# Optimization experiments

Hardware: AMD Instinct MI355X
Metric: run time of the kernel (lower is better)

The kernel has to match this reference:

```python
import jax, jax.numpy as jnp
import numpy as np

B, T, I, H, O = 128, 1024, 128, 1024, 128

def setup_inputs() -> dict:
    key = jax.random.key(0)
    ks = jax.random.split(key, 11)
    s = 1.0 / np.sqrt(H)  # torch default LSTM init scale
    return {
        "x": jax.random.normal(ks[0], (B, T, I), jnp.float32),
        "sequence_length": jax.random.randint(ks[1], (B,), 0, T, jnp.int64 if jax.config.jax_enable_x64 else jnp.int32),
        "hn": jax.random.normal(ks[2], (B, H), jnp.float32),
        "cn": jax.random.normal(ks[3], (B, H), jnp.float32),
        "output_t": jax.random.normal(ks[4], (B, O), jnp.float32),
        "W_ih": jax.random.normal(ks[5], (4 * H, I + O), jnp.float32) * s,
        "W_hh": jax.random.normal(ks[6], (4 * H, H), jnp.float32) * s,
        "b_ih": jax.random.normal(ks[7], (4 * H,), jnp.float32) * s,
        "b_hh": jax.random.normal(ks[8], (4 * H,), jnp.float32) * s,
        "W_out": jax.random.normal(ks[9], (O, H), jnp.float32) * s,
        "b_out": jax.random.normal(ks[10], (O,), jnp.float32) * s,
    }

def reference(x, sequence_length, hn, cn, output_t, W_ih, W_hh, b_ih, b_hh, W_out, b_out):
    # eval mode (self.training=False): no dropout applied
    Tn = x.shape[1]
    Hd = hn.shape[-1]
    # masks[t, b] = 1.0 if sequence_length[b] > t
    masks = (jnp.arange(Tn)[:, None] < sequence_length[None, :]).astype(x.dtype)  # [T, B]
    xs = jnp.transpose(x, (1, 0, 2))  # [T, B, I]
    bias = b_ih + b_hh

    def step(carry, inp):
        h, c, out_t = carry
        xt, m = inp                      # xt [B,I], m [B]
        m = m[:, None]                   # [B,1]
        lstm_in = jnp.concatenate([xt * m, out_t], axis=-1)  # [B, I+O]
        gates = lstm_in @ W_ih.T + h @ W_hh.T + bias          # [B, 4H]
        i_g, f_g, g_g, o_g = jnp.split(gates, 4, axis=-1)     # torch gate order i,f,g,o
        i_g = jax.nn.sigmoid(i_g)
        f_g = jax.nn.sigmoid(f_g)
        g_g = jnp.tanh(g_g)
        o_g = jax.nn.sigmoid(o_g)
        c = f_g * c + i_g * g_g
        h = o_g * jnp.tanh(c)
        out_t = h @ W_out.T + b_out      # [B, O]
        return (h, c, out_t), out_t * m

    (_, _, _), ys = jax.lax.scan(step, (hn, cn, output_t), (xs, masks))
    return jnp.transpose(ys, (1, 0, 2))  # [B, T, O]
```

## Files before the change

### kernel.cpp

```cpp
#include <hip/hip_runtime.h>
#include <stdint.h>

#define Tn 1024
#define In 128

typedef __attribute__((ext_vector_type(8))) short short8;
typedef __attribute__((ext_vector_type(4))) float f32x4;
typedef unsigned long long u64;

#define WS_WFRAG  0ull
#define WS_WOUT   (WS_WFRAG + 10485760ull)
#define WS_Z0     (WS_WOUT + 262144ull)
#define WS_HBUF   (WS_Z0 + 32768ull)
#define WS_BIAS   (WS_HBUF + 524288ull)
#define WS_CNT    (WS_BIAS + 16384ull)

__device__ __forceinline__ unsigned short f2bf(float f) {
  unsigned u = __builtin_bit_cast(unsigned, f);
  return (unsigned short)((u + 0x7FFFu + ((u >> 16) & 1u)) >> 16);
}
__device__ __forceinline__ float fast_sig(float v) {
  float e = __builtin_amdgcn_exp2f(-1.44269504089f * v);
  return __builtin_amdgcn_rcpf(1.0f + e);
}
__device__ __forceinline__ float fast_tanh(float v) {
  float a = fabsf(v);
  float e = __builtin_amdgcn_exp2f(-2.88539008178f * a);
  float r = (1.0f - e) * __builtin_amdgcn_rcpf(1.0f + e);
  return copysignf(r, v);
}

__global__ void k_wfrag(const float* __restrict__ Wih, const float* __restrict__ Whh,
                        const float* __restrict__ Wout, char* __restrict__ ws) {
  const int u = blockIdx.x, nt = blockIdx.y, kt = blockIdx.z;
  const int lane = threadIdx.x;
  const int col = lane & 15, quad = lane >> 4;
  const int r = nt * 16 + col;
  const int g = r >> 5, jj = r & 31;
  const int n = g * 1024 + u * 32 + jj;
  float v[8];
  if (kt < 32) {
    const int k = kt * 32 + quad * 8;
    #pragma unroll
    for (int e = 0; e < 8; e++) v[e] = Whh[(size_t)n * 1024 + k + e];
    const float* wo = Wih + (size_t)n * 256 + 128;
    for (int o = 0; o < 128; o++) {
      const float wv = wo[o];
      const float* wr = Wout + (size_t)o * 1024 + k;
      #pragma unroll
      for (int e = 0; e < 8; e++) v[e] = fmaf(wv, wr[e], v[e]);
    }
  } else if (kt < 36) {
    const int k = (kt - 32) * 32 + quad * 8;
    #pragma unroll
    for (int e = 0; e < 8; e++) v[e] = Wih[(size_t)n * 256 + k + e];
  } else {
    const int o = (kt - 36) * 32 + quad * 8;
    #pragma unroll
    for (int e = 0; e < 8; e++) v[e] = Wih[(size_t)n * 256 + 128 + o + e];
  }
  short8 pk;
  #pragma unroll
  for (int e = 0; e < 8; e++) pk[e] = (short)f2bf(v[e]);
  *(short8*)(ws + WS_WFRAG + ((size_t)((u * 8 + nt) * 40 + kt) * 64 + lane) * 16) = pk;
}

__global__ void k_misc(const float* __restrict__ Wout, const float* __restrict__ hn,
                       const float* __restrict__ out_t, const float* __restrict__ bout,
                       const float* __restrict__ bih, const float* __restrict__ bhh,
                       const float* __restrict__ Wih, float* __restrict__ outp,
                       char* __restrict__ ws) {
  const int blk = blockIdx.x, lane = threadIdx.x;
  const int col = lane & 15, quad = lane >> 4;
  if (blk < 256) {
    const int u = blk >> 5, kt = blk & 31;
    const int o = u * 16 + col, j0 = kt * 32 + quad * 8;
    short8 pk;
    #pragma unroll
    for (int e = 0; e < 8; e++) pk[e] = (short)f2bf(Wout[(size_t)o * 1024 + j0 + e]);
    *(short8*)(ws + WS_WOUT + ((size_t)(u * 32 + kt) * 64 + lane) * 16) = pk;
  } else if (blk < 512) {
    const int t2 = blk - 256;
    const int mm = t2 >> 5, kt = t2 & 31;
    const int b = mm * 16 + col, j0 = kt * 32 + quad * 8;
    short8 pk;
    #pragma unroll
    for (int e = 0; e < 8; e++) pk[e] = (short)f2bf(hn[(size_t)b * 1024 + j0 + e]);
    *(short8*)(ws + WS_HBUF + ((size_t)((8 + mm) * 32 + kt) * 64 + lane) * 16) = pk;
  } else if (blk < 544) {
    const int t2 = blk - 512;
    const int mm = t2 >> 2, kz = t2 & 3;
    const int b = mm * 16 + col;
    const int o0 = kz * 32 + quad * 8;
    float acc[8];
    #pragma unroll
    for (int e = 0; e < 8; e++) acc[e] = out_t[(size_t)b * 128 + o0 + e] - bout[o0 + e];
    for (int j = 0; j < 1024; j += 4) {
      const f32x4 h4 = *(const f32x4*)(hn + (size_t)b * 1024 + j);
      #pragma unroll
      for (int e = 0; e < 8; e++) {
        const f32x4 w4 = *(const f32x4*)(Wout + (size_t)(o0 + e) * 1024 + j);
        acc[e] -= h4[0] * w4[0] + h4[1] * w4[1] + h4[2] * w4[2] + h4[3] * w4[3];
      }
    }
    short8 pk;
    #pragma unroll
    for (int e = 0; e < 8; e++) pk[e] = (short)f2bf(acc[e]);
    *(short8*)(ws + WS_Z0 + ((size_t)(mm * 4 + kz) * 64 + lane) * 16) = pk;
  } else if (blk < 608) {
    const int n = (blk - 544) * 64 + lane;
    float v = bih[n] + bhh[n];
    const float* wo = Wih + (size_t)n * 256 + 128;
    for (int o = 0; o < 128; o++) v = fmaf(wo[o], bout[o], v);
    ((float*)(ws + WS_BIAS))[n] = v;
  } else if (blk < 616) {
    int* c = (int*)(ws + WS_CNT);
    const int base = ((blk - 608) * 64 + lane) * 16;
    #pragma unroll
    for (int k = 0; k < 16; k++) c[base + k] = 0;
  } else {
    int* c = (int*)outp;
    #pragma unroll
    for (int k = 0; k < 8; k++) c[lane * 8 + k] = 0;
  }
}

__launch_bounds__(512, 2)
__global__ void k_main(const float* __restrict__ x, const int* __restrict__ seq,
                       const float* __restrict__ cn, const float* __restrict__ b_out,
                       float* __restrict__ out, char* __restrict__ ws) {
  __shared__ short8 a_lds[40 * 64];
  __shared__ float  gates_lds[128 * 20];
  __shared__ short8 htile[64];
  __shared__ float  ysred[8 * 16 * 20];
  __shared__ float  bias_lds[128];
  __shared__ int    seq_lds[16];

  const int tid  = threadIdx.x;
  const int lane = tid & 63;
  const int w    = tid >> 6;
  const int wg   = blockIdx.x;

  int* cnt = (int*)(ws + WS_CNT);

  int m_, u_, fast_;
  {
    int* ids = (int*)ysred;
    int* scr = (int*)out;
    if (tid == 0) {
      int myxcd;
      asm volatile("s_getreg_b32 %0, hwreg(HW_REG_XCC_ID)" : "=s"(myxcd));
      myxcd &= 7;
      ids[259] = myxcd;
      __hip_atomic_store(&scr[8 + wg], myxcd, __ATOMIC_RELAXED, __HIP_MEMORY_SCOPE_SYSTEM);
      __hip_atomic_fetch_add(&scr[0], 1, __ATOMIC_ACQ_REL, __HIP_MEMORY_SCOPE_SYSTEM);
      while (__hip_atomic_load(&scr[0], __ATOMIC_ACQUIRE, __HIP_MEMORY_SCOPE_SYSTEM) < 256) {}
    }
    __syncthreads();
    if (tid < 256)
      ids[tid] = __hip_atomic_load(&scr[8 + tid], __ATOMIC_RELAXED,
                                   __HIP_MEMORY_SCOPE_SYSTEM) & 7;
    __syncthreads();
    if (tid == 0) {
      const int myxcd = ids[259];
      int cx[8] = {0, 0, 0, 0, 0, 0, 0, 0};
      int rank = 0;
      for (int i = 0; i < 256; i++) {
        const int xi = ids[i];
        cx[xi]++;
        if (xi == myxcd && i < wg) rank++;
      }
      bool bal = true;
      for (int k = 0; k < 8; k++) bal = bal && (cx[k] == 32);
      ids[256] = bal ? myxcd : (wg & 7);
      ids[257] = bal ? rank : (wg >> 3);
      ids[258] = bal ? 1 : 0;
      __hip_atomic_fetch_add(&scr[1], 1, __ATOMIC_ACQ_REL, __HIP_MEMORY_SCOPE_SYSTEM);
      while (__hip_atomic_load(&scr[1], __ATOMIC_ACQUIRE, __HIP_MEMORY_SCOPE_SYSTEM) < 256) {}
    }
    __syncthreads();
    m_ = ids[256]; u_ = ids[257]; fast_ = ids[258];
    __syncthreads();
  }
  const int  m     = m_;
  const int  u     = u_;
  const bool fastp = (fast_ != 0);

  const char* wfrag = ws + WS_WFRAG;
  const char* woutf = ws + WS_WOUT;
  char* hbuf  = ws + WS_HBUF;
  const float* bias2 = (const float*)(ws + WS_BIAS);

  short8 bfr[40];
  {
    const char* base = wfrag + ((size_t)(u * 8 + w) * 40 * 64) * 16 + (size_t)lane * 16;
    #pragma unroll
    for (int kt = 0; kt < 40; kt++) bfr[kt] = *(const short8*)(base + (size_t)kt * 1024);
  }
  if (tid < 16) seq_lds[tid] = seq[m * 16 + tid];
  if (tid < 128) {
    const int g = tid >> 5, jj = tid & 31;
    bias_lds[tid] = bias2[g * 1024 + u * 32 + jj];
  }
  const int b_loc  = tid & 15;
  const int jj_loc = tid >> 4;
  float c_reg = cn[(size_t)(m * 16 + b_loc) * 1024 + u * 32 + jj_loc];
  __syncthreads();

  #pragma unroll 1
  for (int tt = 0; tt <= Tn; tt++) {
    if (tt < Tn && tid < 256) {
      const int kt4 = tid >> 6, ln = tid & 63;
      const int b = ln & 15, quad = ln >> 4;
      const int i0 = kt4 * 32 + quad * 8;
      const float* xp = x + ((size_t)(m * 16 + b) * Tn + tt) * In + i0;
      const float mk = (tt < seq_lds[b]) ? 1.0f : 0.0f;
      const f32x4 x0 = *(const f32x4*)xp;
      const f32x4 x1 = *(const f32x4*)(xp + 4);
      short8 pk;
      pk[0] = (short)f2bf(x0[0] * mk); pk[1] = (short)f2bf(x0[1] * mk);
      pk[2] = (short)f2bf(x0[2] * mk); pk[3] = (short)f2bf(x0[3] * mk);
      pk[4] = (short)f2bf(x1[0] * mk); pk[5] = (short)f2bf(x1[1] * mk);
      pk[6] = (short)f2bf(x1[2] * mk); pk[7] = (short)f2bf(x1[3] * mk);
      a_lds[(32 + kt4) * 64 + ln] = pk;
    }
    if (tt == 0 && tid < 256) {
      const int kz = tid >> 6, ln = tid & 63;
      a_lds[(36 + kz) * 64 + ln] =
          *(const short8*)(ws + WS_Z0 + ((size_t)(m * 4 + kz) * 64 + ln) * 16);
    }
    if (tt >= 1 && tid == 0) {
      while (__hip_atomic_load(&cnt[m * 1024 + (tt - 1)], __ATOMIC_RELAXED,
                               __HIP_MEMORY_SCOPE_SYSTEM) < 32) {}
    }
    __syncthreads();
    {
      const char* srcb = hbuf + (size_t)((((tt + 1) & 1) * 8) + m) * 32768;
      if (fastp && tt >= 1) {
        const f32x4* sp = (const f32x4*)srcb;
        f32x4 t0, t1, t2, t3;
        asm volatile(
            "global_load_dwordx4 %0, %4, off sc0\n\t"
            "global_load_dwordx4 %1, %5, off sc0\n\t"
            "global_load_dwordx4 %2, %6, off sc0\n\t"
            "global_load_dwordx4 %3, %7, off sc0\n\t"
            "s_waitcnt vmcnt(0)"
            : "=&v"(t0), "=&v"(t1), "=&v"(t2), "=&v"(t3)
            : "v"(sp + tid), "v"(sp + 512 + tid), "v"(sp + 1024 + tid),
              "v"(sp + 1536 + tid)
            : "memory");
        f32x4* dst = (f32x4*)a_lds;
        dst[tid] = t0; dst[512 + tid] = t1; dst[1024 + tid] = t2; dst[1536 + tid] = t3;
      } else {
        const u64* src = (const u64*)srcb;
        u64 tmp[8];
        #pragma unroll
        for (int s = 0; s < 8; s++)
          tmp[s] = __hip_atomic_load(&src[s * 512 + tid], __ATOMIC_RELAXED,
                                     __HIP_MEMORY_SCOPE_SYSTEM);
        u64* dst = (u64*)a_lds;
        #pragma unroll
        for (int s = 0; s < 8; s++) dst[s * 512 + tid] = tmp[s];
      }
    }
    __syncthreads();

    if (tt < Tn) {
      const float bias_v = bias_lds[w * 16 + (lane & 15)];
      f32x4 acc0 = {bias_v, bias_v, bias_v, bias_v};
      f32x4 acc1 = {0.f, 0.f, 0.f, 0.f};
      #pragma unroll
      for (int kt = 0; kt < 36; kt += 2) {
        const short8 a0 = a_lds[kt * 64 + lane];
        const short8 a1 = a_lds[(kt + 1) * 64 + lane];
        acc0 = __builtin_amdgcn_mfma_f32_16x16x32_bf16(a0, bfr[kt], acc0, 0, 0, 0);
        acc1 = __builtin_amdgcn_mfma_f32_16x16x32_bf16(a1, bfr[kt + 1], acc1, 0, 0, 0);
      }
      if (tt == 0) {
        #pragma unroll
        for (int kt = 36; kt < 40; kt += 2) {
          const short8 a0 = a_lds[kt * 64 + lane];
          const short8 a1 = a_lds[(kt + 1) * 64 + lane];
          acc0 = __builtin_amdgcn_mfma_f32_16x16x32_bf16(a0, bfr[kt], acc0, 0, 0, 0);
          acc1 = __builtin_amdgcn_mfma_f32_16x16x32_bf16(a1, bfr[kt + 1], acc1, 0, 0, 0);
        }
      }
      {
        const int r = w * 16 + (lane & 15);
        const int bq = (lane >> 4) * 4;
        f32x4 s;
        s[0] = acc0[0] + acc1[0]; s[1] = acc0[1] + acc1[1];
        s[2] = acc0[2] + acc1[2]; s[3] = acc0[3] + acc1[3];
        *(f32x4*)&gates_lds[r * 20 + bq] = s;
      }
      __syncthreads();
      {
        const float Gi = gates_lds[(0 * 32 + jj_loc) * 20 + b_loc];
        const float Gf = gates_lds[(1 * 32 + jj_loc) * 20 + b_loc];
        const float Gg = gates_lds[(2 * 32 + jj_loc) * 20 + b_loc];
        const float Go = gates_lds[(3 * 32 + jj_loc) * 20 + b_loc];
        const float ig = fast_sig(Gi), fg = fast_sig(Gf);
        const float gg = fast_tanh(Gg), og = fast_sig(Go);
        c_reg = fg * c_reg + ig * gg;
        const float h = og * fast_tanh(c_reg);
        ((short*)htile)[(b_loc + 16 * (jj_loc >> 3)) * 8 + (jj_loc & 7)] = (short)f2bf(h);
      }
      __syncthreads();
      if (tid < 64) {
        const short8 v = htile[lane];
        char* dstb = hbuf + (size_t)((tt & 1) * 8 + m) * 32768 + (size_t)u * 1024 +
                     (size_t)lane * 16;
        if (fastp) {
          asm volatile("global_store_dwordx4 %0, %1, off sc0" :: "v"(dstb), "v"(v)
                       : "memory");
        } else {
          u64* dstp = (u64*)dstb;
          const u64* pv = (const u64*)&v;
          __hip_atomic_store(&dstp[0], pv[0], __ATOMIC_RELAXED, __HIP_MEMORY_SCOPE_SYSTEM);
          __hip_atomic_store(&dstp[1], pv[1], __ATOMIC_RELAXED, __HIP_MEMORY_SCOPE_SYSTEM);
        }
        asm volatile("s_waitcnt vmcnt(0)" ::: "memory");
        if (tid == 0)
          __hip_atomic_fetch_add(&cnt[m * 1024 + tt], 1, __ATOMIC_RELAXED,
                                 __HIP_MEMORY_SCOPE_SYSTEM);
      }
    }

    if (u < 8 && tt >= 1) {
      f32x4 yacc = {0.f, 0.f, 0.f, 0.f};
      const char* wob = woutf + ((size_t)(u * 32 + w * 4) * 64 + lane) * 16;
      #pragma unroll
      for (int i = 0; i < 4; i++) {
        const short8 bf = *(const short8*)(wob + (size_t)i * 1024);
        const short8 af = a_lds[(w * 4 + i) * 64 + lane];
        yacc = __builtin_amdgcn_mfma_f32_16x16x32_bf16(af, bf, yacc, 0, 0, 0);
      }
      {
        const int o = lane & 15, bq = (lane >> 4) * 4;
        *(f32x4*)&ysred[(w * 16 + o) * 20 + bq] = yacc;
      }
      __syncthreads();
      if (tid < 256) {
        const int o = tid & 15, b = tid >> 4;
        float s = 0.f;
        #pragma unroll
        for (int q = 0; q < 8; q++) s += ysred[(q * 16 + o) * 20 + b];
        s += b_out[u * 16 + o];
        const float val = ((tt - 1) < seq_lds[b]) ? s : 0.0f;
        out[((size_t)(m * 16 + b) * Tn + (tt - 1)) * 128 + u * 16 + o] = val;
      }
      __syncthreads();
    }
  }
}

extern "C" void kernel_launch(void* const* d_in, const int* in_sizes, int n_in,
                              void* d_out, int out_size, void* d_ws, size_t ws_size,
                              hipStream_t stream) {
  (void)in_sizes; (void)n_in; (void)out_size; (void)ws_size;
  const float* x    = (const float*)d_in[0];
  const int*   seq  = (const int*)d_in[1];
  const float* hn   = (const float*)d_in[2];
  const float* cn   = (const float*)d_in[3];
  const float* outt = (const float*)d_in[4];
  const float* Wih  = (const float*)d_in[5];
  const float* Whh  = (const float*)d_in[6];
  const float* bih  = (const float*)d_in[7];
  const float* bhh  = (const float*)d_in[8];
  const float* Wout = (const float*)d_in[9];
  const float* bout = (const float*)d_in[10];
  float* out = (float*)d_out;
  char* ws = (char*)d_ws;

  hipLaunchKernelGGL(k_wfrag, dim3(32, 8, 40), dim3(64), 0, stream, Wih, Whh, Wout, ws);
  hipLaunchKernelGGL(k_misc, dim3(617), dim3(64), 0, stream, Wout, hn, outt, bout,
                     bih, bhh, Wih, out, ws);
  void* args[] = {(void*)&x, (void*)&seq, (void*)&cn, (void*)&bout, (void*)&out, (void*)&ws};
  hipLaunchCooperativeKernel((const void*)k_main, dim3(256), dim3(512), args, 0, stream);
}
```

Measured before the change: 3.207 ms.

## Split K across waves so each A fragment feeds four MFMA column tiles

Repartitions the per-step gate GEMM so each wave owns a quarter of the K dimension and four 16-column output tiles instead of one column tile over all of K. Each A fragment loaded from LDS is reused across four independent MFMA accumulators, which cuts LDS reads per wave and gives four independent dependency chains in place of two. The cost is a larger partial-sum buffer in LDS and a four-way reduction in the activation phase, which adds LDS traffic and shared memory pressure on a latency-bound serial recurrence.

```diff
diff --git a/kernel.cpp b/kernel.cpp
--- a/kernel.cpp
+++ b/kernel.cpp
@@ -130,7 +130,7 @@
                        const float* __restrict__ cn, const float* __restrict__ b_out,
                        float* __restrict__ out, char* __restrict__ ws) {
   __shared__ short8 a_lds[40 * 64];
-  __shared__ float  gates_lds[128 * 20];
+  __shared__ float  pbuf[4 * 128 * 20];
   __shared__ short8 htile[64];
   __shared__ float  ysred[8 * 16 * 20];
   __shared__ float  bias_lds[128];
@@ -191,11 +191,22 @@
   char* hbuf  = ws + WS_HBUF;
   const float* bias2 = (const float*)(ws + WS_BIAS);
 
-  short8 bfr[40];
+  const int kg   = w >> 1;
+  const int half = w & 1;
+  const int col16 = lane & 15, bq4 = (lane >> 4) * 4;
+
+  short8 bfr[36];
+  short8 bz[4];
   {
-    const char* base = wfrag + ((size_t)(u * 8 + w) * 40 * 64) * 16 + (size_t)lane * 16;
-    #pragma unroll
-    for (int kt = 0; kt < 40; kt++) bfr[kt] = *(const short8*)(base + (size_t)kt * 1024);
+    #pragma unroll
+    for (int j = 0; j < 4; j++) {
+      #pragma unroll
+      for (int kk = 0; kk < 9; kk++)
+        bfr[j * 9 + kk] = *(const short8*)(wfrag +
+            ((size_t)((u * 8 + half * 4 + j) * 40 + kg * 9 + kk) * 64 + lane) * 16);
+      bz[j] = *(const short8*)(wfrag +
+          ((size_t)((u * 8 + half * 4 + j) * 40 + 36 + kg) * 64 + lane) * 16);
+    }
   }
   if (tid < 16) seq_lds[tid] = seq[m * 16 + tid];
   if (tid < 128) {
@@ -266,39 +277,52 @@
     __syncthreads();
 
     if (tt < Tn) {
-      const float bias_v = bias_lds[w * 16 + (lane & 15)];
-      f32x4 acc0 = {bias_v, bias_v, bias_v, bias_v};
-      f32x4 acc1 = {0.f, 0.f, 0.f, 0.f};
+      f32x4 acc0, acc1, acc2, acc3;
+      if (kg == 0) {
+        const float b0 = bias_lds[(half * 4 + 0) * 16 + col16];
+        const float b1 = bias_lds[(half * 4 + 1) * 16 + col16];
+        const float b2 = bias_lds[(half * 4 + 2) * 16 + col16];
+        const float b3 = bias_lds[(half * 4 + 3) * 16 + col16];
+        acc0 = {b0, b0, b0, b0}; acc1 = {b1, b1, b1, b1};
+        acc2 = {b2, b2, b2, b2}; acc3 = {b3, b3, b3, b3};
+      } else {
+        acc0 = {0.f, 0.f, 0.f, 0.f}; acc1 = {0.f, 0.f, 0.f, 0.f};
+        acc2 = {0.f, 0.f, 0.f, 0.f}; acc3 = {0.f, 0.f, 0.f, 0.f};
+      }
       #pragma unroll
-      for (int kt = 0; kt < 36; kt += 2) {
-        const short8 a0 = a_lds[kt * 64 + lane];
-        const short8 a1 = a_lds[(kt + 1) * 64 + lane];
-        acc0 = __builtin_amdgcn_mfma_f32_16x16x32_bf16(a0, bfr[kt], acc0, 0, 0, 0);
-        acc1 = __builtin_amdgcn_mfma_f32_16x16x32_bf16(a1, bfr[kt + 1], acc1, 0, 0, 0);
+      for (int kk = 0; kk < 9; kk++) {
+        const short8 a = a_lds[(kg * 9 + kk) * 64 + lane];
+        acc0 = __builtin_amdgcn_mfma_f32_16x16x32_bf16(a, bfr[0 * 9 + kk], acc0, 0, 0, 0);
+        acc1 = __builtin_amdgcn_mfma_f32_16x16x32_bf16(a, bfr[1 * 9 + kk], acc1, 0, 0, 0);
+        acc2 = __builtin_amdgcn_mfma_f32_16x16x32_bf16(a, bfr[2 * 9 + kk], acc2, 0, 0, 0);
+        acc3 = __builtin_amdgcn_mfma_f32_16x16x32_bf16(a, bfr[3 * 9 + kk], acc3, 0, 0, 0);
       }
       if (tt == 0) {
-        #pragma unroll
-        for (int kt = 36; kt < 40; kt += 2) {
-          const short8 a0 = a_lds[kt * 64 + lane];
-          const short8 a1 = a_lds[(kt + 1) * 64 + lane];
-          acc0 = __builtin_amdgcn_mfma_f32_16x16x32_bf16(a0, bfr[kt], acc0, 0, 0, 0);
-          acc1 = __builtin_amdgcn_mfma_f32_16x16x32_bf16(a1, bfr[kt + 1], acc1, 0, 0, 0);
-        }
+        const short8 a = a_lds[(36 + kg) * 64 + lane];
+        acc0 = __builtin_amdgcn_mfma_f32_16x16x32_bf16(a, bz[0], acc0, 0, 0, 0);
+        acc1 = __builtin_amdgcn_mfma_f32_16x16x32_bf16(a, bz[1], acc1, 0, 0, 0);
+        acc2 = __builtin_amdgcn_mfma_f32_16x16x32_bf16(a, bz[2], acc2, 0, 0, 0);
+        acc3 = __builtin_amdgcn_mfma_f32_16x16x32_bf16(a, bz[3], acc3, 0, 0, 0);
       }
       {
-        const int r = w * 16 + (lane & 15);
-        const int bq = (lane >> 4) * 4;
-        f32x4 s;
-        s[0] = acc0[0] + acc1[0]; s[1] = acc0[1] + acc1[1];
-        s[2] = acc0[2] + acc1[2]; s[3] = acc0[3] + acc1[3];
-        *(f32x4*)&gates_lds[r * 20 + bq] = s;
+        const int rb = kg * 128 + (half * 4) * 16 + col16;
+        *(f32x4*)&pbuf[(size_t)(rb +  0) * 20 + bq4] = acc0;
+        *(f32x4*)&pbuf[(size_t)(rb + 16) * 20 + bq4] = acc1;
+        *(f32x4*)&pbuf[(size_t)(rb + 32) * 20 + bq4] = acc2;
+        *(f32x4*)&pbuf[(size_t)(rb + 48) * 20 + bq4] = acc3;
       }
       __syncthreads();
       {
-        const float Gi = gates_lds[(0 * 32 + jj_loc) * 20 + b_loc];
-        const float Gf = gates_lds[(1 * 32 + jj_loc) * 20 + b_loc];
-        const float Gg = gates_lds[(2 * 32 + jj_loc) * 20 + b_loc];
-        const float Go = gates_lds[(3 * 32 + jj_loc) * 20 + b_loc];
+        const int r0 = 0 * 32 + jj_loc, r1 = 1 * 32 + jj_loc;
+        const int r2 = 2 * 32 + jj_loc, r3 = 3 * 32 + jj_loc;
+        const float Gi = pbuf[(0 * 128 + r0) * 20 + b_loc] + pbuf[(1 * 128 + r0) * 20 + b_loc]
+                       + pbuf[(2 * 128 + r0) * 20 + b_loc] + pbuf[(3 * 128 + r0) * 20 + b_loc];
+        const float Gf = pbuf[(0 * 128 + r1) * 20 + b_loc] + pbuf[(1 * 128 + r1) * 20 + b_loc]
+                       + pbuf[(2 * 128 + r1) * 20 + b_loc] + pbuf[(3 * 128 + r1) * 20 + b_loc];
+        const float Gg = pbuf[(0 * 128 + r2) * 20 + b_loc] + pbuf[(1 * 128 + r2) * 20 + b_loc]
+                       + pbuf[(2 * 128 + r2) * 20 + b_loc] + pbuf[(3 * 128 + r2) * 20 + b_loc];
+        const float Go = pbuf[(0 * 128 + r3) * 20 + b_loc] + pbuf[(1 * 128 + r3) * 20 + b_loc]
+                       + pbuf[(2 * 128 + r3) * 20 + b_loc] + pbuf[(3 * 128 + r3) * 20 + b_loc];
         const float ig = fast_sig(Gi), fg = fast_sig(Gf);
         const float gg = fast_tanh(Gg), og = fast_sig(Go);
         c_reg = fg * c_reg + ig * gg;
```

Result: slower. 3.484 ms (+8.6%).
